# Kernel optimization log

Measured on AMD Instinct MI355X. Metric: run time of the kernel, lower is better.

The kernel has to match this reference:

```python
import jax, jax.numpy as jnp
import numpy as np

N_NODES = 1048576
N_GRAPHS = 4096
NODES_PER_GRAPH = N_NODES // N_GRAPHS
N_EDGES = 8388608
F_IN = 16
HID = 32


def _glorot(k, shp):
    return jax.random.normal(k, shp, jnp.float32) * np.float32(np.sqrt(2.0 / (shp[-2] + shp[-1])))


def setup_inputs() -> dict:
    key = jax.random.key(0)
    ks = jax.random.split(key, 8)
    d = F_IN + HID  # DCRNN gate convs act on cat([X, H])
    return {
        "x": jax.random.normal(ks[0], (N_NODES, F_IN), jnp.float32),
        "edge_index": jax.random.randint(ks[1], (2, N_EDGES), 0, N_NODES),
        "edge_weight": jax.random.uniform(ks[2], (N_EDGES,), jnp.float32),
        "batch": jnp.repeat(jnp.arange(N_GRAPHS), NODES_PER_GRAPH),
        "W_z": _glorot(ks[3], (2, 1, d, HID)),
        "b_z": jnp.zeros((HID,), jnp.float32),
        "W_r": _glorot(ks[4], (2, 1, d, HID)),
        "b_r": jnp.zeros((HID,), jnp.float32),
        "W_h": _glorot(ks[5], (2, 1, d, HID)),
        "b_h": jnp.zeros((HID,), jnp.float32),
        "W_lin": _glorot(ks[6], (HID, 1)),
        "b_lin": jnp.zeros((1,), jnp.float32),
    }


def _dconv_k1(X, W, b):
    # torch_geometric_temporal DConv with K=1: the diffusion loop never runs,
    # so H = X @ W[0,0] + X @ W[1,0] + b (edge_index/edge_weight unused).
    return X @ (W[0, 0] + W[1, 0]) + b


def reference(x, edge_index, edge_weight, batch, W_z, b_z, W_r, b_r, W_h, b_h, W_lin, b_lin):
    del edge_index, edge_weight  # mathematically unused when K=1
    h0 = jnp.zeros((x.shape[0], HID), x.dtype)  # DCRNN hidden state default
    xh = jnp.concatenate([x, h0], axis=1)
    Z = jax.nn.sigmoid(_dconv_k1(xh, W_z, b_z))
    R = jax.nn.sigmoid(_dconv_k1(xh, W_r, b_r))
    xhr = jnp.concatenate([x, h0 * R], axis=1)
    H_tilde = jnp.tanh(_dconv_k1(xhr, W_h, b_h))
    H = Z * h0 + (1.0 - Z) * H_tilde  # (N, 32)
    h = jax.nn.relu(H)
    h = h @ W_lin + b_lin  # (N, 1)
    # global_mean_pool over per-node graph ids
    sums = jax.ops.segment_sum(h, batch, num_segments=N_GRAPHS)
    cnts = jax.ops.segment_sum(jnp.ones((h.shape[0], 1), h.dtype), batch, num_segments=N_GRAPHS)
    return sums / jnp.maximum(cnts, 1.0)  # (N_GRAPHS, 1)
```

## Files before the change

### kernel.cpp

```cpp
#include <hip/hip_runtime.h>

#define N_GRAPHS  4096
#define NPG       256
#define F_IN      16
#define HID       32
#define LOG2E     1.4426950408889634f

#define WS_FLOATS 609

typedef _Float16 half8  __attribute__((ext_vector_type(8)));
typedef float    f32x16 __attribute__((ext_vector_type(16)));

#if __has_builtin(__builtin_amdgcn_exp2f)
#define EXP2(x) __builtin_amdgcn_exp2f(x)
#else
#define EXP2(x) exp2f(x)
#endif

union FragU { uint4 u; half8 h; };

typedef const __attribute__((address_space(1))) void* gptr_t;
typedef __attribute__((address_space(3))) void*       lptr_t;

__device__ __forceinline__ uint4 make_frag32(int f, int l,
    const float* __restrict__ Wz, const float* __restrict__ Wh)
{
    const int col = l & 31, p = l >> 5;
    const float s = (f == 0) ? LOG2E : 2.0f * LOG2E;
    const float* W = (f == 0) ? Wz : Wh;
    FragU u;
#pragma unroll
    for (int j = 0; j < 8; ++j) {
        const int k = p * 8 + j;
        u.h[j] = (_Float16)((W[k * 32 + col] + W[1536 + k * 32 + col]) * s);
    }
    return u.u;
}

__global__ __launch_bounds__(256) void prep_kernel(
    const float* __restrict__ Wz, const float* __restrict__ bz,
    const float* __restrict__ Wh, const float* __restrict__ bh,
    const float* __restrict__ Wlin, const float* __restrict__ blin,
    float* __restrict__ w)
{
    const int t = threadIdx.x;
    if (t < 128) ((uint4*)w)[t] = make_frag32(t >> 6, t & 63, Wz, Wh);
    if (t < HID) {
        w[512 + t] = bz[t] * LOG2E;
        w[544 + t] = bh[t] * (2.0f * LOG2E);
        w[576 + t] = Wlin[t];
    }
    if (t == 0) w[608] = blin[0];
}

__device__ __forceinline__ float gate_term(float az, float ah, float wl, float osum)
{
    const float e1 = EXP2(az);
    const float e2 = EXP2(fminf(ah, 126.0f));
    const float r  = __builtin_amdgcn_rcpf((1.0f + e1) * (e2 + 1.0f));
    float v = (e2 - 1.0f) * r;
    v = v > 0.0f ? v : 0.0f;
    return fmaf(v, wl, osum);
}

__device__ __forceinline__ float tile32(float4 c0, float4 c1,
    half8 Bz, half8 Bh, float bzl, float bhl, float wll, float osum)
{
    const float xf[8] = { c0.x, c0.y, c0.z, c0.w, c1.x, c1.y, c1.z, c1.w };
    half8 Ah, Al;
#pragma unroll
    for (int j = 0; j < 8; ++j) {
        const _Float16 h = (_Float16)xf[j];
        Ah[j] = h;
        Al[j] = (_Float16)(xf[j] - (float)h);
    }
    f32x16 accZ, accH;
#pragma unroll
    for (int i = 0; i < 16; ++i) { accZ[i] = bzl; accH[i] = bhl; }
    accZ = __builtin_amdgcn_mfma_f32_32x32x16_f16(Ah, Bz, accZ, 0, 0, 0);
    accH = __builtin_amdgcn_mfma_f32_32x32x16_f16(Ah, Bh, accH, 0, 0, 0);
    accZ = __builtin_amdgcn_mfma_f32_32x32x16_f16(Al, Bz, accZ, 0, 0, 0);
    accH = __builtin_amdgcn_mfma_f32_32x32x16_f16(Al, Bh, accH, 0, 0, 0);
#pragma unroll
    for (int i = 0; i < 16; ++i)
        osum = gate_term(accZ[i], accH[i], wll, osum);
    return osum;
}

__device__ __forceinline__ float gcn_halfgraph(const float* __restrict__ x,
                                               const float* __restrict__ w,
                                               float* __restrict__ xs_wave,
                                               int g, int half, int lane)
{
    const int col = lane & 31, p = lane >> 5;

    const int gu = col * 16 + p * 8;
    const float* gbase = x + ((size_t)g * NPG + half * 128) * F_IN;

#pragma unroll
    for (int tau = 0; tau < 4; ++tau) {
        const float* src = gbase + tau * 512 + gu;
        __builtin_amdgcn_global_load_lds((gptr_t)(src),
                                         (lptr_t)(xs_wave + tau * 512), 16, 0, 0);
        __builtin_amdgcn_global_load_lds((gptr_t)(src + 4),
                                         (lptr_t)(xs_wave + tau * 512 + 256), 16, 0, 0);
    }

    const uint4* bq = (const uint4*)w;
    FragU uz, uh;
    uz.u = bq[lane];
    uh.u = bq[64 + lane];
    const float bzl = w[512 + col];
    const float bhl = w[544 + col];
    const float wll = w[576 + col];

    asm volatile("s_waitcnt vmcnt(0)" ::: "memory");
    __builtin_amdgcn_sched_barrier(0);

    float osum = 0.0f;
#pragma unroll
    for (int tau = 0; tau < 4; ++tau) {
        const float4 c0 = *(const float4*)(xs_wave + tau * 512 + lane * 4);
        const float4 c1 = *(const float4*)(xs_wave + tau * 512 + 256 + lane * 4);
        osum = tile32(c0, c1, uz.h, uh.h, bzl, bhl, wll, osum);
    }

#pragma unroll
    for (int off = 32; off > 0; off >>= 1)
        osum += __shfl_down(osum, off, 64);
    return osum;
}

__device__ __forceinline__ void gcn_body(const float* __restrict__ x,
                                         const float* __restrict__ w,
                                         float* __restrict__ xs,
                                         float* __restrict__ part,
                                         float* __restrict__ out, int b, int t)
{
    const int wv = t >> 6, lane = t & 63;
    const int g = b * 2 + (wv >> 1);
    const float osum = gcn_halfgraph(x, w, xs + wv * 2048, g, wv & 1, lane);

    if (lane == 0) part[wv] = osum;
    __syncthreads();
    if (t == 0) {
        const float bl = w[608];
        out[b * 2]     = (part[0] + part[1]) * (1.0f / (float)NPG) + bl;
        out[b * 2 + 1] = (part[2] + part[3]) * (1.0f / (float)NPG) + bl;
    }
}

__global__ __launch_bounds__(256, 4) void gcn_main(
    const float* __restrict__ x, const float* __restrict__ w, float* __restrict__ out)
{
    __shared__ __attribute__((aligned(16))) float xs[4 * 2048];
    __shared__ float part[4];
    gcn_body(x, w, xs, part, out, blockIdx.x, threadIdx.x);
}

__global__ __launch_bounds__(256, 4) void gcn_main_lds(
    const float* __restrict__ x,
    const float* __restrict__ Wz, const float* __restrict__ bz,
    const float* __restrict__ Wh, const float* __restrict__ bh,
    const float* __restrict__ Wlin, const float* __restrict__ blin,
    float* __restrict__ out)
{
    __shared__ __attribute__((aligned(16))) float w[WS_FLOATS];
    __shared__ __attribute__((aligned(16))) float xs[4 * 2048];
    __shared__ float part[4];
    const int t = threadIdx.x;
    if (t < 128) ((uint4*)w)[t] = make_frag32(t >> 6, t & 63, Wz, Wh);
    if (t < HID) {
        w[512 + t] = bz[t] * LOG2E;
        w[544 + t] = bh[t] * (2.0f * LOG2E);
        w[576 + t] = Wlin[t];
    }
    if (t == 0) w[608] = blin[0];
    __syncthreads();
    gcn_body(x, w, xs, part, out, blockIdx.x, t);
}

extern "C" void kernel_launch(void* const* d_in, const int* in_sizes, int n_in,
                              void* d_out, int out_size, void* d_ws, size_t ws_size,
                              hipStream_t stream)
{
    const float* x    = (const float*)d_in[0];
    const float* Wz   = (const float*)d_in[4];
    const float* bz   = (const float*)d_in[5];
    const float* Wh   = (const float*)d_in[8];
    const float* bh   = (const float*)d_in[9];
    const float* Wlin = (const float*)d_in[10];
    const float* blin = (const float*)d_in[11];
    float* out = (float*)d_out;

    if (ws_size >= WS_FLOATS * sizeof(float)) {
        float* w = (float*)d_ws;
        prep_kernel<<<1, 256, 0, stream>>>(Wz, bz, Wh, bh, Wlin, blin, w);
        gcn_main<<<N_GRAPHS / 2, 256, 0, stream>>>(x, w, out);
    } else {
        gcn_main_lds<<<N_GRAPHS / 2, 256, 0, stream>>>(x, Wz, bz, Wh, bh, Wlin, blin, out);
    }
}
```

Baseline: 170.5 us.

## Fuse weight prep into main kernel and pipeline tile waits per load

```diff
diff --git a/kernel.cpp b/kernel.cpp
--- a/kernel.cpp
+++ b/kernel.cpp
@@ -5,8 +5,6 @@
 #define F_IN      16
 #define HID       32
 #define LOG2E     1.4426950408889634f
-
-#define WS_FLOATS 609
 
 typedef _Float16 half8  __attribute__((ext_vector_type(8)));
 typedef float    f32x16 __attribute__((ext_vector_type(16)));
@@ -17,41 +15,8 @@
 #define EXP2(x) exp2f(x)
 #endif
 
-union FragU { uint4 u; half8 h; };
-
 typedef const __attribute__((address_space(1))) void* gptr_t;
 typedef __attribute__((address_space(3))) void*       lptr_t;
-
-__device__ __forceinline__ uint4 make_frag32(int f, int l,
-    const float* __restrict__ Wz, const float* __restrict__ Wh)
-{
-    const int col = l & 31, p = l >> 5;
-    const float s = (f == 0) ? LOG2E : 2.0f * LOG2E;
-    const float* W = (f == 0) ? Wz : Wh;
-    FragU u;
-#pragma unroll
-    for (int j = 0; j < 8; ++j) {
-        const int k = p * 8 + j;
-        u.h[j] = (_Float16)((W[k * 32 + col] + W[1536 + k * 32 + col]) * s);
-    }
-    return u.u;
-}
-
-__global__ __launch_bounds__(256) void prep_kernel(
-    const float* __restrict__ Wz, const float* __restrict__ bz,
-    const float* __restrict__ Wh, const float* __restrict__ bh,
-    const float* __restrict__ Wlin, const float* __restrict__ blin,
-    float* __restrict__ w)
-{
-    const int t = threadIdx.x;
-    if (t < 128) ((uint4*)w)[t] = make_frag32(t >> 6, t & 63, Wz, Wh);
-    if (t < HID) {
-        w[512 + t] = bz[t] * LOG2E;
-        w[544 + t] = bh[t] * (2.0f * LOG2E);
-        w[576 + t] = Wlin[t];
-    }
-    if (t == 0) w[608] = blin[0];
-}
 
 __device__ __forceinline__ float gate_term(float az, float ah, float wl, float osum)
 {
@@ -87,97 +52,91 @@
     return osum;
 }
 
-__device__ __forceinline__ float gcn_halfgraph(const float* __restrict__ x,
-                                               const float* __restrict__ w,
-                                               float* __restrict__ xs_wave,
-                                               int g, int half, int lane)
-{
-    const int col = lane & 31, p = lane >> 5;
-
-    const int gu = col * 16 + p * 8;
-    const float* gbase = x + ((size_t)g * NPG + half * 128) * F_IN;
-
-#pragma unroll
-    for (int tau = 0; tau < 4; ++tau) {
-        const float* src = gbase + tau * 512 + gu;
-        __builtin_amdgcn_global_load_lds((gptr_t)(src),
-                                         (lptr_t)(xs_wave + tau * 512), 16, 0, 0);
-        __builtin_amdgcn_global_load_lds((gptr_t)(src + 4),
-                                         (lptr_t)(xs_wave + tau * 512 + 256), 16, 0, 0);
-    }
-
-    const uint4* bq = (const uint4*)w;
-    FragU uz, uh;
-    uz.u = bq[lane];
-    uh.u = bq[64 + lane];
-    const float bzl = w[512 + col];
-    const float bhl = w[544 + col];
-    const float wll = w[576 + col];
-
-    asm volatile("s_waitcnt vmcnt(0)" ::: "memory");
-    __builtin_amdgcn_sched_barrier(0);
-
-    float osum = 0.0f;
-#pragma unroll
-    for (int tau = 0; tau < 4; ++tau) {
-        const float4 c0 = *(const float4*)(xs_wave + tau * 512 + lane * 4);
-        const float4 c1 = *(const float4*)(xs_wave + tau * 512 + 256 + lane * 4);
-        osum = tile32(c0, c1, uz.h, uh.h, bzl, bhl, wll, osum);
-    }
-
-#pragma unroll
-    for (int off = 32; off > 0; off >>= 1)
-        osum += __shfl_down(osum, off, 64);
-    return osum;
-}
-
-__device__ __forceinline__ void gcn_body(const float* __restrict__ x,
-                                         const float* __restrict__ w,
-                                         float* __restrict__ xs,
-                                         float* __restrict__ part,
-                                         float* __restrict__ out, int b, int t)
-{
-    const int wv = t >> 6, lane = t & 63;
-    const int g = b * 2 + (wv >> 1);
-    const float osum = gcn_halfgraph(x, w, xs + wv * 2048, g, wv & 1, lane);
-
-    if (lane == 0) part[wv] = osum;
-    __syncthreads();
-    if (t == 0) {
-        const float bl = w[608];
-        out[b * 2]     = (part[0] + part[1]) * (1.0f / (float)NPG) + bl;
-        out[b * 2 + 1] = (part[2] + part[3]) * (1.0f / (float)NPG) + bl;
-    }
-}
-
-__global__ __launch_bounds__(256, 4) void gcn_main(
-    const float* __restrict__ x, const float* __restrict__ w, float* __restrict__ out)
-{
-    __shared__ __attribute__((aligned(16))) float xs[4 * 2048];
-    __shared__ float part[4];
-    gcn_body(x, w, xs, part, out, blockIdx.x, threadIdx.x);
-}
-
-__global__ __launch_bounds__(256, 4) void gcn_main_lds(
+__global__ __launch_bounds__(256, 4) void gcn_fused(
     const float* __restrict__ x,
     const float* __restrict__ Wz, const float* __restrict__ bz,
     const float* __restrict__ Wh, const float* __restrict__ bh,
     const float* __restrict__ Wlin, const float* __restrict__ blin,
     float* __restrict__ out)
 {
-    __shared__ __attribute__((aligned(16))) float w[WS_FLOATS];
     __shared__ __attribute__((aligned(16))) float xs[4 * 2048];
     __shared__ float part[4];
-    const int t = threadIdx.x;
-    if (t < 128) ((uint4*)w)[t] = make_frag32(t >> 6, t & 63, Wz, Wh);
-    if (t < HID) {
-        w[512 + t] = bz[t] * LOG2E;
-        w[544 + t] = bh[t] * (2.0f * LOG2E);
-        w[576 + t] = Wlin[t];
+    const int t = threadIdx.x, wv = t >> 6, lane = t & 63;
+    const int col = lane & 31, p = lane >> 5;
+    const int g = blockIdx.x * 2 + (wv >> 1), half = wv & 1;
+    float* xs_wave = xs + wv * 2048;
+
+    float z0[8], z1[8], h0[8], h1[8];
+#pragma unroll
+    for (int j = 0; j < 8; ++j) {
+        const int k = p * 8 + j;
+        z0[j] = Wz[k * 32 + col];
+        z1[j] = Wz[1536 + k * 32 + col];
+        h0[j] = Wh[k * 32 + col];
+        h1[j] = Wh[1536 + k * 32 + col];
     }
-    if (t == 0) w[608] = blin[0];
+    const float bz_raw = bz[col], bh_raw = bh[col];
+    const float wll = Wlin[col], bl = blin[0];
+    __builtin_amdgcn_sched_barrier(0);
+
+    const int gu = col * 16 + p * 8;
+    const float* gbase = x + ((size_t)g * NPG + half * 128) * F_IN;
+#pragma unroll
+    for (int tau = 0; tau < 4; ++tau) {
+        const float* src = gbase + tau * 512 + gu;
+        __builtin_amdgcn_global_load_lds((gptr_t)src,
+                                         (lptr_t)(xs_wave + tau * 512), 16, 0, 0);
+        __builtin_amdgcn_global_load_lds((gptr_t)(src + 4),
+                                         (lptr_t)(xs_wave + tau * 512 + 256), 16, 0, 0);
+    }
+    __builtin_amdgcn_sched_barrier(0);
+
+    half8 Bz, Bh;
+#pragma unroll
+    for (int j = 0; j < 8; ++j) {
+        Bz[j] = (_Float16)((z0[j] + z1[j]) * LOG2E);
+        Bh[j] = (_Float16)((h0[j] + h1[j]) * (2.0f * LOG2E));
+    }
+    const float bzl = bz_raw * LOG2E;
+    const float bhl = bh_raw * (2.0f * LOG2E);
+
+    float osum = 0.0f;
+
+    asm volatile("s_waitcnt vmcnt(6)" ::: "memory");
+    {
+        const float4 c0 = *(const float4*)(xs_wave + 0 * 512 + lane * 4);
+        const float4 c1 = *(const float4*)(xs_wave + 0 * 512 + 256 + lane * 4);
+        osum = tile32(c0, c1, Bz, Bh, bzl, bhl, wll, osum);
+    }
+    asm volatile("s_waitcnt vmcnt(4)" ::: "memory");
+    {
+        const float4 c0 = *(const float4*)(xs_wave + 1 * 512 + lane * 4);
+        const float4 c1 = *(const float4*)(xs_wave + 1 * 512 + 256 + lane * 4);
+        osum = tile32(c0, c1, Bz, Bh, bzl, bhl, wll, osum);
+    }
+    asm volatile("s_waitcnt vmcnt(2)" ::: "memory");
+    {
+        const float4 c0 = *(const float4*)(xs_wave + 2 * 512 + lane * 4);
+        const float4 c1 = *(const float4*)(xs_wave + 2 * 512 + 256 + lane * 4);
+        osum = tile32(c0, c1, Bz, Bh, bzl, bhl, wll, osum);
+    }
+    asm volatile("s_waitcnt vmcnt(0)" ::: "memory");
+    {
+        const float4 c0 = *(const float4*)(xs_wave + 3 * 512 + lane * 4);
+        const float4 c1 = *(const float4*)(xs_wave + 3 * 512 + 256 + lane * 4);
+        osum = tile32(c0, c1, Bz, Bh, bzl, bhl, wll, osum);
+    }
+
+#pragma unroll
+    for (int off = 32; off > 0; off >>= 1)
+        osum += __shfl_down(osum, off, 64);
+
+    if (lane == 0) part[wv] = osum;
     __syncthreads();
-    gcn_body(x, w, xs, part, out, blockIdx.x, t);
+    if (t == 0) {
+        out[blockIdx.x * 2]     = (part[0] + part[1]) * (1.0f / (float)NPG) + bl;
+        out[blockIdx.x * 2 + 1] = (part[2] + part[3]) * (1.0f / (float)NPG) + bl;
+    }
 }
 
 extern "C" void kernel_launch(void* const* d_in, const int* in_sizes, int n_in,
@@ -192,12 +151,7 @@
     const float* Wlin = (const float*)d_in[10];
     const float* blin = (const float*)d_in[11];
     float* out = (float*)d_out;
+    (void)d_ws; (void)ws_size;
 
-    if (ws_size >= WS_FLOATS * sizeof(float)) {
-        float* w = (float*)d_ws;
-        prep_kernel<<<1, 256, 0, stream>>>(Wz, bz, Wh, bh, Wlin, blin, w);
-        gcn_main<<<N_GRAPHS / 2, 256, 0, stream>>>(x, w, out);
-    } else {
-        gcn_main_lds<<<N_GRAPHS / 2, 256, 0, stream>>>(x, Wz, bz, Wh, bh, Wlin, blin, out);
-    }
+    gcn_fused<<<N_GRAPHS / 2, 256, 0, stream>>>(x, Wz, bz, Wh, bh, Wlin, blin, out);
 }
```

Result: faster. 166.7 us (-2.2%).
